# Performance work log

Hardware: AMD Instinct MI355X
Metric: run time of the kernel (lower is better)

The kernel has to match this reference:

```python
import jax, jax.numpy as jnp
import numpy as np

B, N, C, CODE, DIRB = 4, 321408, 3, 7, 2
K_PRE, K_POST = 1000, 300
IOU_THR, SCORE_THR, DIR_OFFSET = 0.5, 0.05, 0.0
POST_RANGE = np.array([0.0, -39.68, -5.0, 69.12, 39.68, 5.0], dtype=np.float32)


def setup_inputs() -> dict:
    key = jax.random.key(0)
    k1, k2, k3, k4 = jax.random.split(key, 4)
    box_preds = jax.random.normal(k1, (B, N, CODE), jnp.float32) * 0.3
    # shift logits down so sigmoid scores straddle the 0.05 threshold realistically
    cls_preds = jax.random.normal(k2, (B, N, C), jnp.float32) * 2.0 - 2.0
    dir_preds = jax.random.normal(k3, (B, N, DIRB), jnp.float32)
    ka, kb, kc = jax.random.split(k4, 3)
    xy = jax.random.uniform(ka, (N, 2), jnp.float32) * jnp.array([69.12, 79.36], jnp.float32) + jnp.array([0.0, -39.68], jnp.float32)
    z = jnp.full((N, 1), -1.0, jnp.float32)
    dims = jax.random.uniform(kb, (N, 3), jnp.float32, minval=1.0, maxval=4.0)
    rot = jax.random.randint(kc, (N, 1), 0, 2).astype(jnp.float32) * np.float32(np.pi / 2)
    anchors = jnp.concatenate([xy, z, dims, rot], axis=-1)
    return {"box_preds": box_preds, "cls_preds": cls_preds, "dir_preds": dir_preds, "anchors": anchors}


def _decode(deltas, anchors):
    # SECOND / PointPillars GroundBox3dCoder decode. anchors: [x,y,z,w,l,h,r]
    xa, ya, za, wa, la, ha, ra = (anchors[..., i] for i in range(7))
    xt, yt, zt, wt, lt, ht, rt = (deltas[..., i] for i in range(7))
    za = za + ha * 0.5
    diag = jnp.sqrt(la * la + wa * wa)
    xg = xt * diag + xa
    yg = yt * diag + ya
    zg = zt * ha + za
    wg = jnp.exp(wt) * wa
    lg = jnp.exp(lt) * la
    hg = jnp.exp(ht) * ha
    zg = zg - hg * 0.5
    rg = rt + ra
    return jnp.stack([xg, yg, zg, wg, lg, hg, rg], axis=-1)


def _nms_single(boxes7, scores, valid):
    # boxes_for_nms = box[:, [0,1,3,4,-1]] -> rotated (x,y,w,l,r); standup AABB of corners
    x, y, w, l, r = boxes7[:, 0], boxes7[:, 1], boxes7[:, 3], boxes7[:, 4], boxes7[:, 6]
    c, s = jnp.abs(jnp.cos(r)), jnp.abs(jnp.sin(r))
    hx = 0.5 * (w * c + l * s)   # half-extent of rotated corners along x
    hy = 0.5 * (w * s + l * c)
    x1, x2, y1, y2 = x - hx, x + hx, y - hy, y + hy
    area = (x2 - x1) * (y2 - y1)
    ix = jnp.clip(jnp.minimum(x2[:, None], x2[None, :]) - jnp.maximum(x1[:, None], x1[None, :]), 0.0)
    iy = jnp.clip(jnp.minimum(y2[:, None], y2[None, :]) - jnp.maximum(y1[:, None], y1[None, :]), 0.0)
    inter = ix * iy
    union = area[:, None] + area[None, :] - inter
    iou = jnp.where(union > 0, inter / jnp.maximum(union, 1e-12), 0.0)
    iou = jax.lax.stop_gradient(iou)
    idxs = jnp.arange(K_PRE)

    def body(keep, i):
        sup = keep[i] & (iou[i] > IOU_THR) & (idxs > i)
        return keep & ~sup, None

    keep, _ = jax.lax.scan(body, valid, idxs)
    rank = jnp.cumsum(keep) - 1                       # rank among kept (score order)
    pos = jnp.argsort(jnp.where(keep, rank, K_PRE))   # stable: kept-in-order first
    sel = pos[:K_POST]
    return sel, keep[sel]


def reference(box_preds, cls_preds, dir_preds, anchors):
    decoded = _decode(box_preds, anchors[None, :, :])          # [B,N,7]
    probs = jax.nn.sigmoid(cls_preds)                          # [B,N,C]
    top_scores = probs.max(axis=-1)
    top_labels = probs.argmax(axis=-1).astype(jnp.int32)
    dir_labels = dir_preds.argmax(axis=-1).astype(jnp.int32)
    valid = top_scores >= SCORE_THR
    sc_masked = jnp.where(valid, top_scores, -1.0)
    sc_k, idx = jax.lax.top_k(sc_masked, K_PRE)                # [B,K_PRE]
    boxes_k = jnp.take_along_axis(decoded, idx[..., None], axis=1)
    labels_k = jnp.take_along_axis(top_labels, idx, axis=1)
    dir_k = jnp.take_along_axis(dir_labels, idx, axis=1)
    valid_k = sc_k >= SCORE_THR
    sel, keep = jax.vmap(_nms_single)(boxes_k, sc_k, valid_k)  # [B,K_POST]
    boxes = jnp.take_along_axis(boxes_k, sel[..., None], axis=1)
    scores = jnp.take_along_axis(sc_k, sel, axis=1)
    labels = jnp.take_along_axis(labels_k, sel, axis=1)
    dirs = jnp.take_along_axis(dir_k, sel, axis=1)
    # direction flip: add pi where predicted direction disagrees with yaw sign
    opp = ((boxes[..., 6] - DIR_OFFSET) > 0) ^ (dirs == 1)
    r_fixed = boxes[..., 6] + jnp.where(opp, np.float32(np.pi), np.float32(0.0))
    boxes = jnp.concatenate([boxes[..., :6], r_fixed[..., None]], axis=-1)
    # post center-range filter
    lo = jnp.asarray(POST_RANGE[:3])
    hi = jnp.asarray(POST_RANGE[3:])
    in_range = jnp.all(boxes[..., :3] >= lo, axis=-1) & jnp.all(boxes[..., :3] <= hi, axis=-1)
    valid_out = keep & in_range
    boxes = jnp.where(valid_out[..., None], boxes, 0.0)
    scores = jnp.where(valid_out, scores, 0.0)
    labels = jnp.where(valid_out, labels, 0)
    return boxes, labels, scores, valid_out
```

## Files before the change

### kernel.cpp

```cpp
#include <hip/hip_runtime.h>
#include <stdint.h>

typedef unsigned long long u64;
typedef unsigned int u32;

#define BB 4
#define NN 321408
#define K_PRE 1000
#define K_POST 300
#define CAP 4096
#define NW 16
#define SCORE_THR 0.05f
#define IOU_THR 0.5f
#define SB 314
#define CH2 1024
#define NBINS 576
#define BIN0 0xBD4Cu
#define RED 4
#define RCH 79

__device__ __forceinline__ float sigm(float x) { return 1.0f / (1.0f + expf(-x)); }

__device__ __forceinline__ u32 mkkey(float mx) {
    float s = sigm(mx);
    return (s >= SCORE_THR) ? (__float_as_uint(s) | 0x80000000u) : 0u;
}

__global__ void k_score_hist(const float* __restrict__ cls, u32* __restrict__ key, u32* __restrict__ bh) {
    __shared__ u32 h1[NBINS], h2[NBINS];
    int bb = blockIdx.x, tid = threadIdx.x;
    int b = bb / SB, c = bb % SB;
    for (int i = tid; i < NBINS; i += 256) h1[i] = 0;
    __syncthreads();
    int a0 = c * CH2 + tid * 4;
    if (a0 < NN) {
        const float4* c4 = (const float4*)(cls + ((size_t)b * NN + a0) * 3);
        float4 v0 = c4[0], v1 = c4[1], v2 = c4[2];
        uint4 o;
        o.x = mkkey(fmaxf(v0.x, fmaxf(v0.y, v0.z)));
        o.y = mkkey(fmaxf(v0.w, fmaxf(v1.x, v1.y)));
        o.z = mkkey(fmaxf(v1.z, fmaxf(v1.w, v2.x)));
        o.w = mkkey(fmaxf(v2.y, fmaxf(v2.z, v2.w)));
        *((uint4*)(key + (size_t)b * NN + a0)) = o;
        if (o.x) atomicAdd(&h1[min((o.x >> 16) - BIN0, (u32)(NBINS - 1))], 1u);
        if (o.y) atomicAdd(&h1[min((o.y >> 16) - BIN0, (u32)(NBINS - 1))], 1u);
        if (o.z) atomicAdd(&h1[min((o.z >> 16) - BIN0, (u32)(NBINS - 1))], 1u);
        if (o.w) atomicAdd(&h1[min((o.w >> 16) - BIN0, (u32)(NBINS - 1))], 1u);
    }
    __syncthreads();
    u32* src = h1; u32* dst = h2;
    for (int off = 1; off < NBINS; off <<= 1) {
        for (int i = tid; i < NBINS; i += 256)
            dst[i] = src[i] + ((i + off < NBINS) ? src[i + off] : 0u);
        __syncthreads();
        u32* t = src; src = dst; dst = t;
    }
    for (int i = tid; i < NBINS; i += 256) bh[(size_t)bb * NBINS + i] = src[i];
}

__global__ __launch_bounds__(64) void k_red(const u32* __restrict__ bh, u32* __restrict__ part) {
    int blk = blockIdx.x, tid = threadIdx.x;
    int b = blk / (RED * 9);
    int r = (blk / 9) % RED;
    int g = blk % 9;
    int f = g * 64 + tid;
    int s0 = r * RCH, s1 = s0 + RCH; if (s1 > SB) s1 = SB;
    const u32* base = bh + (size_t)(b * SB + s0) * NBINS + f;
    u32 acc = 0;
    int n = s1 - s0;
    #pragma unroll 8
    for (int s = 0; s < n; ++s) acc += base[(size_t)s * NBINS];
    part[(size_t)(b * RED + r) * NBINS + f] = acc;
}

__global__ __launch_bounds__(512) void k_scanoff(const u32* __restrict__ part, const u32* __restrict__ bh,
                                                 u32* __restrict__ thr, u32* __restrict__ boff,
                                                 u32* __restrict__ cnt) {
    __shared__ u32 tot[NBINS];
    __shared__ u32 s[512];
    __shared__ u32 sT, starg;
    int b = blockIdx.x, tid = threadIdx.x;
    for (int f = tid; f < NBINS; f += 512) {
        u32 x = 0;
        #pragma unroll
        for (int r = 0; r < RED; ++r) x += part[(size_t)(b * RED + r) * NBINS + f];
        tot[f] = x;
    }
    __syncthreads();
    if (tid == 0) {
        u32 tv = tot[0];
        starg = (tv < K_PRE) ? tv : K_PRE;
        if (starg == 0) { sT = 0x10000u; thr[b] = 0x10000u; }
    }
    __syncthreads();
    u32 target = starg;
    if (target > 0) {
        for (int f = tid; f < NBINS; f += 512) {
            u32 cge = tot[f];
            u32 cnx = (f + 1 < NBINS) ? tot[f + 1] : 0u;
            if (cge >= target && cnx < target) { sT = BIN0 + (u32)f; thr[b] = BIN0 + (u32)f; }
        }
    }
    __syncthreads();
    u32 v = 0;
    if (target > 0 && tid < SB) {
        u32 T = sT - BIN0;
        v = bh[(size_t)(b * SB + tid) * NBINS + T];
    }
    s[tid] = v;
    __syncthreads();
    for (int o = 1; o < 512; o <<= 1) {
        u32 x = (tid >= o) ? s[tid - o] : 0u;
        __syncthreads();
        s[tid] += x;
        __syncthreads();
    }
    if (tid < SB) boff[b * SB + tid] = s[tid] - v;
    if (tid == 511) cnt[b] = s[511];
}

__global__ void k_scatter(const u32* __restrict__ key, const u32* __restrict__ thr,
                          const u32* __restrict__ boff, u64* __restrict__ cand) {
    __shared__ u32 wtot[4];
    int bb = blockIdx.x, tid = threadIdx.x;
    int b = bb / SB, c = bb % SB;
    u32 T = thr[b];
    int a0 = c * CH2 + tid * 4;
    uint4 kk = make_uint4(0u, 0u, 0u, 0u);
    if (a0 < NN) kk = *((const uint4*)(key + (size_t)b * NN + a0));
    u32 ks[4] = {kk.x, kk.y, kk.z, kk.w};
    u32 f[4];
    #pragma unroll
    for (int e = 0; e < 4; ++e) f[e] = (u32)((ks[e] != 0) && ((ks[e] >> 16) >= T));
    u32 tc = f[0] + f[1] + f[2] + f[3];
    int lane = tid & 63, wv = tid >> 6;
    u32 x = tc;
    #pragma unroll
    for (int o = 1; o < 64; o <<= 1) {
        u32 y = __shfl_up(x, o);
        if (lane >= o) x += y;
    }
    if (lane == 63) wtot[wv] = x;
    __syncthreads();
    u32 base = 0;
    u32 w0 = wtot[0], w1 = wtot[1], w2 = wtot[2];
    if (wv > 0) base += w0;
    if (wv > 1) base += w1;
    if (wv > 2) base += w2;
    u32 pos = boff[bb] + base + x - tc;
    u64* cb = cand + (size_t)b * CAP;
    #pragma unroll
    for (int e = 0; e < 4; ++e) {
        if (f[e]) {
            if (pos < CAP) cb[pos] = ((u64)(~ks[e]) << 32) | (u64)(a0 + e);
            ++pos;
        }
    }
}

__global__ __launch_bounds__(256) void k_rankdec(const u32* __restrict__ cnt, const u64* __restrict__ cand,
                                                 const float* __restrict__ boxp, const float* __restrict__ cls,
                                                 const float* __restrict__ dirp, const float* __restrict__ anch,
                                                 float* __restrict__ tks, u32* __restrict__ meta,
                                                 float* __restrict__ box7, float* __restrict__ cor) {
    __shared__ u64 ck[CAP];
    int blk = blockIdx.x, tid = threadIdx.x;
    int b = blk >> 4, rb = blk & 15;
    u32 nc = cnt[b]; if (nc > CAP) nc = CAP;
    int ci = rb * 256 + tid;
    if (rb * 256 >= (int)nc && rb * 256 >= K_PRE) return;
    const u64* cb = cand + (size_t)b * CAP;
    for (int i = tid; i < (int)nc; i += 256) ck[i] = cb[i];
    __syncthreads();

    int rank = -1; u32 idx = 0xFFFFFFFFu;
    if (ci < (int)nc) {
        u64 my = ck[ci];
        u32 r = 0;
        int j = 0;
        int nlim = (int)nc & ~15;
        for (; j < nlim; j += 16) {
            u64 v0 = ck[j+0], v1 = ck[j+1], v2 = ck[j+2], v3 = ck[j+3];
            u64 v4 = ck[j+4], v5 = ck[j+5], v6 = ck[j+6], v7 = ck[j+7];
            u64 v8 = ck[j+8], v9 = ck[j+9], va = ck[j+10], vb = ck[j+11];
            u64 vc = ck[j+12], vd = ck[j+13], ve = ck[j+14], vf = ck[j+15];
            r += (u32)(v0 < my) + (u32)(v1 < my) + (u32)(v2 < my) + (u32)(v3 < my)
               + (u32)(v4 < my) + (u32)(v5 < my) + (u32)(v6 < my) + (u32)(v7 < my)
               + (u32)(v8 < my) + (u32)(v9 < my) + (u32)(va < my) + (u32)(vb < my)
               + (u32)(vc < my) + (u32)(vd < my) + (u32)(ve < my) + (u32)(vf < my);
        }
        for (; j < (int)nc; ++j) r += (u32)(ck[j] < my);
        if (r < K_PRE) { rank = (int)r; idx = (u32)my; }
    } else if (ci < K_PRE) {
        rank = ci;
    }
    if (rank < 0) return;

    float ob[7] = {0,0,0,0,0,0,0};
    float c5[5] = {0,0,0,0,0};
    float sc = 0.f; u32 mt = 0;
    if (idx != 0xFFFFFFFFu) {
        const float* A = anch + (size_t)idx * 7;
        const float* D = boxp + ((size_t)b * NN + idx) * 7;
        float xa=A[0], ya=A[1], za=A[2], wa=A[3], la=A[4], ha=A[5], ra=A[6];
        float xt=D[0], yt=D[1], zt=D[2], wt=D[3], lt=D[4], ht=D[5], rt=D[6];
        za = za + ha * 0.5f;
        float diag = sqrtf(la * la + wa * wa);
        float xg = xt * diag + xa;
        float yg = yt * diag + ya;
        float zg = zt * ha + za;
        float wg = expf(wt) * wa;
        float lg = expf(lt) * la;
        float hg = expf(ht) * ha;
        zg = zg - hg * 0.5f;
        float rg = rt + ra;
        ob[0]=xg; ob[1]=yg; ob[2]=zg; ob[3]=wg; ob[4]=lg; ob[5]=hg; ob[6]=rg;
        float cr = fabsf(cosf(rg)), sr = fabsf(sinf(rg));
        float hx = 0.5f * (wg * cr + lg * sr);
        float hy = 0.5f * (wg * sr + lg * cr);
        float x1 = xg - hx, x2 = xg + hx, y1 = yg - hy, y2 = yg + hy;
        c5[0]=x1; c5[1]=x2; c5[2]=y1; c5[3]=y2; c5[4]=(x2-x1)*(y2-y1);
        const float* cc = cls + ((size_t)b * NN + idx) * 3;
        float p0 = sigm(cc[0]), p1 = sigm(cc[1]), p2 = sigm(cc[2]);
        int lbl = 0; float best = p0;
        if (p1 > best) { best = p1; lbl = 1; }
        if (p2 > best) { best = p2; lbl = 2; }
        sc = best;
        const float* dd = dirp + ((size_t)b * NN + idx) * 2;
        int dl = (dd[1] > dd[0]) ? 1 : 0;
        mt = (u32)lbl | ((u32)dl << 8) | (1u << 16);
    }
    size_t t = (size_t)b * K_PRE + rank;
    tks[t] = sc; meta[t] = mt;
    #pragma unroll
    for (int j = 0; j < 7; ++j) box7[t * 7 + j] = ob[j];
    #pragma unroll
    for (int j = 0; j < 5; ++j) cor[t * 5 + j] = c5[j];
}

__global__ __launch_bounds__(256) void k_maskT(const float* __restrict__ cor, u64* __restrict__ maskT) {
    __shared__ float s4[(K_PRE + 16) * 4];
    __shared__ float sA[K_PRE + 16];
    int blk = blockIdx.x;
    int b = blk / 63, jb = blk % 63;
    int tid = threadIdx.x;
    const float4* C4 = (const float4*)(cor + (size_t)b * K_PRE * 5);
    for (int q = tid; q < (K_PRE * 5) / 4; q += 256) {
        float4 v = C4[q];
        int t0 = q * 4;
        #pragma unroll
        for (int e = 0; e < 4; ++e) {
            int t = t0 + e;
            int i = t / 5, k = t - i * 5;
            float val = (e == 0) ? v.x : (e == 1) ? v.y : (e == 2) ? v.z : v.w;
            int ip = i + (i >> 6);
            if (k < 4) s4[ip * 4 + k] = val; else sA[ip] = val;
        }
    }
    __syncthreads();
    int w = tid & 15, jl = tid >> 4;
    int j = jb * 16 + jl;
    if (j >= K_PRE) return;
    int jp = j + (j >> 6);
    float x1 = s4[jp*4+0], x2 = s4[jp*4+1], y1 = s4[jp*4+2], y2 = s4[jp*4+3], ar = sA[jp];
    u64 m = 0;
    int i0 = w * 64;
    if (i0 < j) {
        int iend = j - i0; if (iend > 64) iend = 64;
        for (int ii = 0; ii < iend; ++ii) {
            int i = i0 + ii;
            int ip = i + (i >> 6);
            float4 bx = *(const float4*)&s4[ip * 4];
            float ai = sA[ip];
            float ix = fminf(x2, bx.y) - fmaxf(x1, bx.x); ix = fmaxf(ix, 0.f);
            float iy = fminf(y2, bx.w) - fmaxf(y1, bx.z); iy = fmaxf(iy, 0.f);
            float inter = ix * iy;
            float uni = ai + ar - inter;
            float iou = (uni > 0.f) ? inter / fmaxf(uni, 1e-12f) : 0.f;
            if (iou > IOU_THR) m |= (1ull << ii);
        }
    }
    maskT[((size_t)b * K_PRE + j) * NW + w] = m;
}

__global__ __launch_bounds__(256) void k_nms_out(const u32* __restrict__ meta, const float* __restrict__ box7,
                                                 const float* __restrict__ tks, const u64* __restrict__ maskT,
                                                 float* __restrict__ out) {
    int b = blockIdx.x; int tid = threadIdx.x;
    __shared__ u64 km_s[16];
    __shared__ int sel_s[K_POST];
    __shared__ int cnt_s;
    if (tid < 16) km_s[tid] = 0ull;
    __syncthreads();
    if (tid < 64) {
        int lane = tid;
        const u32* M = meta + b * K_PRE;
        int cnt = 0; bool done = false;
        for (int c = 0; c < 16; ++c) {
            if (done) break;
            int j = c * 64 + lane;
            int jc = (j < K_PRE) ? j : (K_PRE - 1);
            bool jvalid = (j < K_PRE) && ((M[jc] >> 16) & 1u);
            const u64* colp = maskT + ((size_t)b * K_PRE + jc) * NW;
            u64 cw = 0; u64 supacc = 0;
            #pragma unroll
            for (int w = 0; w < 16; ++w) {
                u64 cv = colp[w];
                supacc |= (cv & km_s[w]);
                if (w == c) cw = cv;
            }
            u64 active = __ballot(jvalid && (supacc == 0ull));
            u64 kmc = 0;
            while (active) {
                int i = __ffsll((unsigned long long)active) - 1;
                if (lane == 0) sel_s[cnt] = c * 64 + i;
                ++cnt;
                if (cnt >= K_POST) { done = true; break; }
                kmc |= (1ull << i);
                u64 supb = __ballot(((cw >> i) & 1ull) != 0ull);
                active &= ~supb;
                active &= ~(1ull << i);
            }
            if (lane == 0) km_s[c] = kmc;
        }
        if (lane == 0) cnt_s = cnt;
    }
    __syncthreads();
    int cnt = cnt_s;
    const u32* M = meta + b * K_PRE;
    const float* BX = box7 + (size_t)b * K_PRE * 7;
    const float* SS = tks + b * K_PRE;
    for (int p = tid; p < K_POST; p += 256) {
        float ob[7] = {0,0,0,0,0,0,0};
        float sc = 0.f, lb = 0.f, vd = 0.f;
        if (p < cnt) {
            int i = sel_s[p];
            float xg = BX[i*7+0], yg = BX[i*7+1], zg = BX[i*7+2];
            bool in_range = (xg >= 0.0f) && (xg <= 69.12f) &&
                            (yg >= -39.68f) && (yg <= 39.68f) &&
                            (zg >= -5.0f) && (zg <= 5.0f);
            if (in_range) {
                u32 mt = M[i];
                int dl = (mt >> 8) & 0xFF;
                float r = BX[i*7+6];
                bool opp = ((r > 0.0f) != (dl == 1));
                float rf = r + (opp ? 3.14159274f : 0.0f);
                ob[0]=xg; ob[1]=yg; ob[2]=zg; ob[3]=BX[i*7+3]; ob[4]=BX[i*7+4]; ob[5]=BX[i*7+5]; ob[6]=rf;
                sc = SS[i]; lb = (float)(mt & 0xFF); vd = 1.0f;
            }
        }
        size_t ro = (size_t)(b * K_POST + p);
        #pragma unroll
        for (int j = 0; j < 7; ++j) out[ro * 7 + j] = ob[j];
        out[(size_t)BB * K_POST * 7 + ro] = lb;
        out[(size_t)BB * K_POST * 8 + ro] = sc;
        out[(size_t)BB * K_POST * 9 + ro] = vd;
    }
}

extern "C" void kernel_launch(void* const* d_in, const int* in_sizes, int n_in,
                              void* d_out, int out_size, void* d_ws, size_t ws_size,
                              hipStream_t stream) {
    const float* boxp = (const float*)d_in[0];
    const float* cls  = (const float*)d_in[1];
    const float* dirp = (const float*)d_in[2];
    const float* anch = (const float*)d_in[3];
    float* out = (float*)d_out;

    char* p = (char*)d_ws;
    u32* key  = (u32*)p; p += (size_t)BB * NN * 4;
    u32* bh   = (u32*)p; p += (size_t)BB * SB * NBINS * 4;
    u32* part = (u32*)p; p += (size_t)BB * RED * NBINS * 4;
    u32* cnt  = (u32*)p; p += 256;
    u32* thr  = (u32*)p; p += 256;
    u32* boff = (u32*)p; p += (size_t)BB * SB * 4 + 256;
    u64* cand = (u64*)p; p += (size_t)BB * CAP * 8;
    float* tks = (float*)p; p += (size_t)BB * K_PRE * 4;
    u32* meta = (u32*)p; p += (size_t)BB * K_PRE * 4;
    float* box7 = (float*)p; p += (size_t)BB * K_PRE * 7 * 4;
    float* cor  = (float*)p; p += (size_t)BB * K_PRE * 5 * 4;
    u64* maskT = (u64*)p; p += (size_t)BB * K_PRE * NW * 8;

    k_score_hist<<<BB * SB, 256, 0, stream>>>(cls, key, bh);
    k_red<<<BB * RED * 9, 64, 0, stream>>>(bh, part);
    k_scanoff<<<BB, 512, 0, stream>>>(part, bh, thr, boff, cnt);
    k_scatter<<<BB * SB, 256, 0, stream>>>(key, thr, boff, cand);
    k_rankdec<<<BB * 16, 256, 0, stream>>>(cnt, cand, boxp, cls, dirp, anch, tks, meta, box7, cor);
    k_maskT<<<BB * 63, 256, 0, stream>>>(cor, maskT);
    k_nms_out<<<BB, 256, 0, stream>>>(meta, box7, tks, maskT, out);
}
```

Baseline: 90.16 us.

## Fold histogram reduction into scan kernel, use wave-shuffle scan, read candidates from global

Removes the separate k_red launch and has k_scanoff sum all 314 per-block histograms itself, so each of the 4 blocks performs a serial sweep of about 180K values. The block-wide offset scan becomes a wave-level shuffle scan plus a small cross-wave prefix, replacing the log-step shared-memory scan with its many barriers. k_rankdec drops its shared-memory candidate staging and reads the candidate array directly from global/cache with an 8-wide unroll. This trades one launch and some barriers for a long serial reduction on only 4 blocks and cache-bound rank counting.

```diff
diff --git a/kernel.cpp b/kernel.cpp
--- a/kernel.cpp
+++ b/kernel.cpp
@@ -16,8 +16,6 @@
 #define CH2 1024
 #define NBINS 576
 #define BIN0 0xBD4Cu
-#define RED 4
-#define RCH 79
 
 __device__ __forceinline__ float sigm(float x) { return 1.0f / (1.0f + expf(-x)); }
 
@@ -58,34 +56,21 @@
     for (int i = tid; i < NBINS; i += 256) bh[(size_t)bb * NBINS + i] = src[i];
 }
 
-__global__ __launch_bounds__(64) void k_red(const u32* __restrict__ bh, u32* __restrict__ part) {
-    int blk = blockIdx.x, tid = threadIdx.x;
-    int b = blk / (RED * 9);
-    int r = (blk / 9) % RED;
-    int g = blk % 9;
-    int f = g * 64 + tid;
-    int s0 = r * RCH, s1 = s0 + RCH; if (s1 > SB) s1 = SB;
-    const u32* base = bh + (size_t)(b * SB + s0) * NBINS + f;
-    u32 acc = 0;
-    int n = s1 - s0;
-    #pragma unroll 8
-    for (int s = 0; s < n; ++s) acc += base[(size_t)s * NBINS];
-    part[(size_t)(b * RED + r) * NBINS + f] = acc;
-}
-
-__global__ __launch_bounds__(512) void k_scanoff(const u32* __restrict__ part, const u32* __restrict__ bh,
-                                                 u32* __restrict__ thr, u32* __restrict__ boff,
-                                                 u32* __restrict__ cnt) {
+__global__ __launch_bounds__(512) void k_scanoff(const u32* __restrict__ bh, u32* __restrict__ thr,
+                                                 u32* __restrict__ boff, u32* __restrict__ cnt) {
     __shared__ u32 tot[NBINS];
-    __shared__ u32 s[512];
+    __shared__ u32 wt[8];
     __shared__ u32 sT, starg;
     int b = blockIdx.x, tid = threadIdx.x;
-    for (int f = tid; f < NBINS; f += 512) {
-        u32 x = 0;
-        #pragma unroll
-        for (int r = 0; r < RED; ++r) x += part[(size_t)(b * RED + r) * NBINS + f];
-        tot[f] = x;
-    }
+    u32 acc0 = 0, acc1 = 0;
+    const u32* base = bh + (size_t)b * SB * NBINS;
+    for (int s = 0; s < SB; ++s) {
+        const u32* row = base + (size_t)s * NBINS;
+        acc0 += row[tid];
+        if (tid < NBINS - 512) acc1 += row[tid + 512];
+    }
+    tot[tid] = acc0;
+    if (tid < NBINS - 512) tot[tid + 512] = acc1;
     __syncthreads();
     if (tid == 0) {
         u32 tv = tot[0];
@@ -107,16 +92,20 @@
         u32 T = sT - BIN0;
         v = bh[(size_t)(b * SB + tid) * NBINS + T];
     }
-    s[tid] = v;
-    __syncthreads();
-    for (int o = 1; o < 512; o <<= 1) {
-        u32 x = (tid >= o) ? s[tid - o] : 0u;
-        __syncthreads();
-        s[tid] += x;
-        __syncthreads();
-    }
-    if (tid < SB) boff[b * SB + tid] = s[tid] - v;
-    if (tid == 511) cnt[b] = s[511];
+    int lane = tid & 63, wv = tid >> 6;
+    u32 x = v;
+    #pragma unroll
+    for (int o = 1; o < 64; o <<= 1) {
+        u32 y = __shfl_up(x, o);
+        if (lane >= o) x += y;
+    }
+    if (lane == 63) wt[wv] = x;
+    __syncthreads();
+    u32 pre = 0;
+    #pragma unroll
+    for (int w = 0; w < 7; ++w) pre += (w < wv) ? wt[w] : 0u;
+    if (tid < SB) boff[b * SB + tid] = pre + x - v;
+    if (tid == 511) cnt[b] = pre + x;
 }
 
 __global__ void k_scatter(const u32* __restrict__ key, const u32* __restrict__ thr,
@@ -163,33 +152,26 @@
                                                  const float* __restrict__ dirp, const float* __restrict__ anch,
                                                  float* __restrict__ tks, u32* __restrict__ meta,
                                                  float* __restrict__ box7, float* __restrict__ cor) {
-    __shared__ u64 ck[CAP];
     int blk = blockIdx.x, tid = threadIdx.x;
     int b = blk >> 4, rb = blk & 15;
     u32 nc = cnt[b]; if (nc > CAP) nc = CAP;
     int ci = rb * 256 + tid;
     if (rb * 256 >= (int)nc && rb * 256 >= K_PRE) return;
     const u64* cb = cand + (size_t)b * CAP;
-    for (int i = tid; i < (int)nc; i += 256) ck[i] = cb[i];
-    __syncthreads();
 
     int rank = -1; u32 idx = 0xFFFFFFFFu;
     if (ci < (int)nc) {
-        u64 my = ck[ci];
+        u64 my = cb[ci];
         u32 r = 0;
         int j = 0;
-        int nlim = (int)nc & ~15;
-        for (; j < nlim; j += 16) {
-            u64 v0 = ck[j+0], v1 = ck[j+1], v2 = ck[j+2], v3 = ck[j+3];
-            u64 v4 = ck[j+4], v5 = ck[j+5], v6 = ck[j+6], v7 = ck[j+7];
-            u64 v8 = ck[j+8], v9 = ck[j+9], va = ck[j+10], vb = ck[j+11];
-            u64 vc = ck[j+12], vd = ck[j+13], ve = ck[j+14], vf = ck[j+15];
+        int nlim = (int)nc & ~7;
+        for (; j < nlim; j += 8) {
+            u64 v0 = cb[j+0], v1 = cb[j+1], v2 = cb[j+2], v3 = cb[j+3];
+            u64 v4 = cb[j+4], v5 = cb[j+5], v6 = cb[j+6], v7 = cb[j+7];
             r += (u32)(v0 < my) + (u32)(v1 < my) + (u32)(v2 < my) + (u32)(v3 < my)
-               + (u32)(v4 < my) + (u32)(v5 < my) + (u32)(v6 < my) + (u32)(v7 < my)
-               + (u32)(v8 < my) + (u32)(v9 < my) + (u32)(va < my) + (u32)(vb < my)
-               + (u32)(vc < my) + (u32)(vd < my) + (u32)(ve < my) + (u32)(vf < my);
-        }
-        for (; j < (int)nc; ++j) r += (u32)(ck[j] < my);
+               + (u32)(v4 < my) + (u32)(v5 < my) + (u32)(v6 < my) + (u32)(v7 < my);
+        }
+        for (; j < (int)nc; ++j) r += (u32)(cb[j] < my);
         if (r < K_PRE) { rank = (int)r; idx = (u32)my; }
     } else if (ci < K_PRE) {
         rank = ci;
@@ -370,7 +352,6 @@
     char* p = (char*)d_ws;
     u32* key  = (u32*)p; p += (size_t)BB * NN * 4;
     u32* bh   = (u32*)p; p += (size_t)BB * SB * NBINS * 4;
-    u32* part = (u32*)p; p += (size_t)BB * RED * NBINS * 4;
     u32* cnt  = (u32*)p; p += 256;
     u32* thr  = (u32*)p; p += 256;
     u32* boff = (u32*)p; p += (size_t)BB * SB * 4 + 256;
@@ -382,8 +363,7 @@
     u64* maskT = (u64*)p; p += (size_t)BB * K_PRE * NW * 8;
 
     k_score_hist<<<BB * SB, 256, 0, stream>>>(cls, key, bh);
-    k_red<<<BB * RED * 9, 64, 0, stream>>>(bh, part);
-    k_scanoff<<<BB, 512, 0, stream>>>(part, bh, thr, boff, cnt);
+    k_scanoff<<<BB, 512, 0, stream>>>(bh, thr, boff, cnt);
     k_scatter<<<BB * SB, 256, 0, stream>>>(key, thr, boff, cand);
     k_rankdec<<<BB * 16, 256, 0, stream>>>(cnt, cand, boxp, cls, dirp, anch, tks, meta, box7, cor);
     k_maskT<<<BB * 63, 256, 0, stream>>>(cor, maskT);
```

Result: slower. 205.6 us (+128.0%).
